# Performance work log

Measured on AMD Instinct MI355X. Metric: run time of the kernel, lower is better.

Reference implementation:

```python
import jax, jax.numpy as jnp
import numpy as np

N_USERS = 50000
N_ENTITIES = 100000
CHANNEL = 64
N_FACTORS = 4
N_REL = 9  # n_relations; weight has N_REL-1 rows
N_EDGES = 1_500_000
NNZ = 800_000
N_HOPS = 2


def _l2_normalize(x, eps=1e-12):
    # matches torch F.normalize(dim=1)
    n = jnp.sqrt(jnp.sum(x * x, axis=1, keepdims=True))
    return x / jnp.maximum(n, eps)


def _distance_correlation(t1, t2):
    # t1, t2: [d] rows of disen_weight_att (d = n_relations-1)
    ch = t1.shape[0]
    t1 = t1[:, None]
    t2 = t2[:, None]
    a_ = (t1 @ t1.T) * 2.0
    b_ = (t2 @ t2.T) * 2.0
    t1s = t1 ** 2
    t2s = t2 ** 2
    a = jnp.sqrt(jnp.maximum(t1s - a_ + t1s.T, 0.0) + 1e-8)
    b = jnp.sqrt(jnp.maximum(t2s - b_ + t2s.T, 0.0) + 1e-8)
    A = a - a.mean(axis=0, keepdims=True) - a.mean(axis=1, keepdims=True) + a.mean()
    B = b - b.mean(axis=0, keepdims=True) - b.mean(axis=1, keepdims=True) + b.mean()
    dcov_AB = jnp.sqrt(jnp.maximum((A * B).sum() / ch ** 2, 0.0) + 1e-8)
    dcov_AA = jnp.sqrt(jnp.maximum((A * A).sum() / ch ** 2, 0.0) + 1e-8)
    dcov_BB = jnp.sqrt(jnp.maximum((B * B).sum() / ch ** 2, 0.0) + 1e-8)
    return dcov_AB / jnp.sqrt(dcov_AA * dcov_BB + 1e-8)


def _cul_cor(disen_weight_att):
    cor = jnp.asarray(0.0, disen_weight_att.dtype)
    for i in range(N_FACTORS):
        for j in range(i + 1, N_FACTORS):
            cor = cor + _distance_correlation(disen_weight_att[i], disen_weight_att[j])
    return cor


def setup_inputs() -> dict:
    key = jax.random.key(0)
    ks = jax.random.split(key, 11)
    return {
        "user_emb": jax.random.normal(ks[0], (N_USERS, CHANNEL), jnp.float32) * 0.1,
        "entity_emb": jax.random.normal(ks[1], (N_ENTITIES, CHANNEL), jnp.float32) * 0.1,
        "latent_emb": jax.random.normal(ks[2], (N_FACTORS, CHANNEL), jnp.float32) * 0.1,
        "weight": jax.random.normal(ks[3], (N_REL - 1, CHANNEL), jnp.float32) * 0.1,
        "disen_weight_att": jax.random.normal(ks[4], (N_FACTORS, N_REL - 1), jnp.float32) * 0.1,
        "interact_vals": jax.random.uniform(ks[5], (NNZ,), jnp.float32),
        "head": jax.random.randint(ks[6], (N_EDGES,), 0, N_ENTITIES),
        "tail": jax.random.randint(ks[7], (N_EDGES,), 0, N_ENTITIES),
        "edge_type": jax.random.randint(ks[8], (N_EDGES,), 1, N_REL),  # in [1, N_REL-1]
        "interact_rows": jax.random.randint(ks[9], (NNZ,), 0, N_USERS),
        "interact_cols": jax.random.randint(ks[10], (NNZ,), 0, N_ENTITIES),
    }


def reference(user_emb, entity_emb, latent_emb, weight, disen_weight_att,
              interact_vals, head, tail, edge_type, interact_rows, interact_cols):
    n_entities = entity_emb.shape[0]
    n_users = user_emb.shape[0]
    cor = _cul_cor(disen_weight_att)

    entity_res = entity_emb
    user_res = user_emb
    ones_e = jnp.ones((head.shape[0],), entity_emb.dtype)
    cnt = jax.ops.segment_sum(ones_e, head, num_segments=n_entities)  # reused: head fixed
    cnt = jnp.maximum(cnt, 1.0)[:, None]

    for _ in range(N_HOPS):
        # KG aggregate: gather tail emb * relation emb, scatter-mean by head
        rel_emb = weight[edge_type - 1]                      # [E, C]
        msg = entity_emb[tail] * rel_emb                     # [E, C]
        entity_agg = jax.ops.segment_sum(msg, head, num_segments=n_entities) / cnt

        # user -> latent factor attention
        score = jax.nn.softmax(user_emb @ latent_emb.T, axis=1)   # [U, F]

        # user aggregate: sparse.mm(interact_mat, entity_emb)
        gathered = interact_vals[:, None] * entity_emb[interact_cols]  # [nnz, C]
        user_agg = jax.ops.segment_sum(gathered, interact_rows, num_segments=n_users)

        disen_weight = jax.nn.softmax(disen_weight_att, axis=-1) @ weight  # [F, C]
        mix = score @ disen_weight                                          # [U, C]
        user_new = user_agg * mix + user_agg

        entity_emb = _l2_normalize(entity_agg)
        user_emb = _l2_normalize(user_new)
        entity_res = entity_res + entity_emb
        user_res = user_res + user_emb

    return entity_res, user_res, cor
```

## Files before the change

kernel.cpp:

```cpp
#include <hip/hip_runtime.h>
#include <math.h>

constexpr int CH         = 64;
constexpr int N_USERS    = 50000;
constexpr int N_ENTITIES = 100000;
constexpr int N_FACTORS  = 4;
constexpr int N_RELM1    = 8;
constexpr int N_EDGES    = 1500000;
constexpr int NNZ        = 800000;

constexpr int NBE        = (N_ENTITIES + 255) / 256;
constexpr int NBU        = (N_USERS + 255) / 256;
constexpr int NBKT       = NBE + NBU;
constexpr int TOTAL      = N_EDGES + NNZ;
constexpr int IPB        = 2048;
constexpr int NBLK       = (TOTAL + IPB - 1) / IPB;
constexpr int ENT_BLK8   = N_ENTITIES / 8;
constexpr int USR_BLK8   = N_USERS / 8;

typedef unsigned int u32;
typedef float __attribute__((ext_vector_type(4))) f32x4;
typedef unsigned int __attribute__((ext_vector_type(4))) u32x4;

__device__ __forceinline__ u32 pack_bf16x2(float a, float b) {
    u32 ua = __float_as_uint(a), ub = __float_as_uint(b);
    u32 ra = (ua + 0x7FFFu + ((ua >> 16) & 1u)) >> 16;
    u32 rb = (ub + 0x7FFFu + ((ub >> 16) & 1u)) >> 16;
    return ra | (rb << 16);
}
__device__ __forceinline__ float bf_lo(u32 v) { return __uint_as_float(v << 16); }
__device__ __forceinline__ float bf_hi(u32 v) { return __uint_as_float(v & 0xFFFF0000u); }

__device__ __forceinline__ float4 nt_ld4f(const float4* p) {
    f32x4 v = __builtin_nontemporal_load((const f32x4*)p);
    return make_float4(v.x, v.y, v.z, v.w);
}
__device__ __forceinline__ void nt_st4f(float4* p, float4 v) {
    f32x4 t; t.x = v.x; t.y = v.y; t.z = v.z; t.w = v.w;
    __builtin_nontemporal_store(t, (f32x4*)p);
}
__device__ __forceinline__ int   nt_ldi(const int* p)   { return __builtin_nontemporal_load(p); }
__device__ __forceinline__ float nt_ldf(const float* p) { return __builtin_nontemporal_load(p); }

__device__ __forceinline__ uint4 gz(const u32* __restrict__ t, int r, int c8, bool v) {
    uint4 x = make_uint4(0u, 0u, 0u, 0u);
    if (v) x = ((const uint4*)t)[r * 8 + c8];
    return x;
}

__device__ __forceinline__ int coarse_bucket(int i, const int* __restrict__ head,
                                             const int* __restrict__ irows) {
    return (i < N_EDGES) ? (head[i] >> 8) : (NBE + (irows[i - N_EDGES] >> 8));
}

__global__ __launch_bounds__(256)
void count_coarse(const int* __restrict__ head, const int* __restrict__ irows,
                  int* __restrict__ H) {
    __shared__ int hist[NBKT];
    for (int j = threadIdx.x; j < NBKT; j += 256) hist[j] = 0;
    __syncthreads();
    int start = blockIdx.x * IPB;
    int end   = min(start + IPB, TOTAL);
    for (int i = start + threadIdx.x; i < end; i += 256)
        atomicAdd(&hist[coarse_bucket(i, head, irows)], 1);
    __syncthreads();
    for (int j = threadIdx.x; j < NBKT; j += 256)
        H[j * NBLK + blockIdx.x] = hist[j];
}

__global__ __launch_bounds__(64)
void scan_hcols(int* __restrict__ H, int* __restrict__ T) {
    int b = blockIdx.x, lane = threadIdx.x;
    int carry = 0;
    for (int c = 0; c < (NBLK + 63) / 64; ++c) {
        int idx = c * 64 + lane;
        int v = (idx < NBLK) ? H[b * NBLK + idx] : 0;
        int incl = v;
        #pragma unroll
        for (int d = 1; d < 64; d <<= 1) {
            int u = __shfl_up(incl, d, 64);
            if (lane >= d) incl += u;
        }
        if (idx < NBLK) H[b * NBLK + idx] = carry + incl - v;
        carry += __shfl(incl, 63, 64);
    }
    if (lane == 0) T[b] = carry;
}

__global__ __launch_bounds__(1024)
void scan_buckets(const int* __restrict__ T, int* __restrict__ Bb) {
    __shared__ int lds[1024];
    int t = threadIdx.x;
    int v = (t < NBKT) ? T[t] : 0;
    lds[t] = v;
    __syncthreads();
    for (int d = 1; d < 1024; d <<= 1) {
        int u = (t >= d) ? lds[t - d] : 0;
        __syncthreads();
        lds[t] += u;
        __syncthreads();
    }
    if (t < NBKT) Bb[t] = lds[t] - v;
    if (t == NBKT - 1) Bb[NBKT] = lds[t];
}

__global__ __launch_bounds__(256)
void scatter_stage(const int* __restrict__ head, const int* __restrict__ tail,
                   const int* __restrict__ etype,
                   const int* __restrict__ irows, const int* __restrict__ icols,
                   const float* __restrict__ ivals,
                   const int* __restrict__ H, const int* __restrict__ Bb,
                   u32* __restrict__ stageE, u32* __restrict__ stageU,
                   float* __restrict__ stageUv) {
    __shared__ int cur[NBKT];
    for (int j = threadIdx.x; j < NBKT; j += 256)
        cur[j] = Bb[j] + H[j * NBLK + blockIdx.x];
    __syncthreads();
    int start = blockIdx.x * IPB;
    int end   = min(start + IPB, TOTAL);
    for (int i = start + threadIdx.x; i < end; i += 256) {
        if (i < N_EDGES) {
            int k   = head[i];
            u32 rec = (u32)tail[i] | ((u32)(etype[i] - 1) << 17) | ((u32)(k & 255) << 20);
            int pos = atomicAdd(&cur[k >> 8], 1);
            stageE[pos] = rec;
        } else {
            int ii  = i - N_EDGES;
            int k   = irows[ii];
            int pos = atomicAdd(&cur[NBE + (k >> 8)], 1) - N_EDGES;
            stageU[pos]  = (u32)icols[ii] | ((u32)(k & 255) << 17);
            stageUv[pos] = ivals[ii];
        }
    }
}

__global__ __launch_bounds__(256)
void bin_fill(const int* __restrict__ Bb,
              const u32* __restrict__ stageE, const u32* __restrict__ stageU,
              const float* __restrict__ stageUv,
              int* __restrict__ offE, int* __restrict__ offU,
              int* __restrict__ elst, int* __restrict__ ucol,
              float* __restrict__ uval) {
    __shared__ int khist[256];
    __shared__ int cur[256];
    int b = blockIdx.x, t = threadIdx.x;
    khist[t] = 0;
    __syncthreads();
    if (b < NBE) {
        int lo = Bb[b], hi = Bb[b + 1];
        for (int i = lo + t; i < hi; i += 256)
            atomicAdd(&khist[(stageE[i] >> 20) & 255], 1);
        __syncthreads();
        int v = khist[t];
        for (int d = 1; d < 256; d <<= 1) {
            int u = (t >= d) ? khist[t - d] : 0;
            __syncthreads();
            khist[t] += u;
            __syncthreads();
        }
        int excl = lo + khist[t] - v;
        int key  = b * 256 + t;
        if (key < N_ENTITIES) offE[key] = excl;
        cur[t] = excl;
        __syncthreads();
        for (int i = lo + t; i < hi; i += 256) {
            u32 s = stageE[i];
            int p = atomicAdd(&cur[(s >> 20) & 255], 1);
            elst[p] = (int)(s & 0xFFFFFu);
        }
        if (b == 0 && t == 0) offE[N_ENTITIES] = N_EDGES;
    } else {
        int lo = Bb[b] - N_EDGES, hi = Bb[b + 1] - N_EDGES;
        for (int i = lo + t; i < hi; i += 256)
            atomicAdd(&khist[(stageU[i] >> 17) & 255], 1);
        __syncthreads();
        int v = khist[t];
        for (int d = 1; d < 256; d <<= 1) {
            int u = (t >= d) ? khist[t - d] : 0;
            __syncthreads();
            khist[t] += u;
            __syncthreads();
        }
        int excl = lo + khist[t] - v;
        int key  = (b - NBE) * 256 + t;
        if (key < N_USERS) offU[key] = excl;
        cur[t] = excl;
        __syncthreads();
        for (int i = lo + t; i < hi; i += 256) {
            u32 s = stageU[i];
            float vv = stageUv[i];
            int p = atomicAdd(&cur[(s >> 17) & 255], 1);
            ucol[p] = (int)(s & 0x1FFFFu);
            uval[p] = vv;
        }
        if (b == NBE && t == 0) offU[N_USERS] = NNZ;
    }
}

__global__ __launch_bounds__(256)
void to_bf16(const float* __restrict__ src, u32* __restrict__ dst, int n2) {
    int i = blockIdx.x * 256 + threadIdx.x;
    if (i < n2) {
        float2 f = ((const float2*)src)[i];
        dst[i] = pack_bf16x2(f.x, f.y);
    }
}

__device__ __forceinline__ void acc_edge(float* acc, uint4 xv, float4 wa, float4 wb) {
    acc[0] += bf_lo(xv.x) * wa.x; acc[1] += bf_hi(xv.x) * wa.y;
    acc[2] += bf_lo(xv.y) * wa.z; acc[3] += bf_hi(xv.y) * wa.w;
    acc[4] += bf_lo(xv.z) * wb.x; acc[5] += bf_hi(xv.z) * wb.y;
    acc[6] += bf_lo(xv.w) * wb.z; acc[7] += bf_hi(xv.w) * wb.w;
}
__device__ __forceinline__ void acc_user(float* acc, uint4 xv, float vv) {
    acc[0] += vv * bf_lo(xv.x); acc[1] += vv * bf_hi(xv.x);
    acc[2] += vv * bf_lo(xv.y); acc[3] += vv * bf_hi(xv.y);
    acc[4] += vv * bf_lo(xv.z); acc[5] += vv * bf_hi(xv.z);
    acc[6] += vv * bf_lo(xv.w); acc[7] += vv * bf_hi(xv.w);
}

template <bool HOP0>
__global__ __launch_bounds__(256)
void hop_pass(const u32* __restrict__ entB,
              const float* __restrict__ usr_in,
              const float* __restrict__ weight, const float* __restrict__ latent,
              const float* __restrict__ dw,
              const int* __restrict__ offE, const int* __restrict__ elst,
              const int* __restrict__ offU, const int* __restrict__ ucol,
              const float* __restrict__ uval,
              u32* __restrict__ AeB_out,
              float* __restrict__ Au_out,
              float* __restrict__ ent_res, float* __restrict__ usr_res,
              const float* __restrict__ ent_base, const float* __restrict__ usr_base) {
    __shared__ float4 w4[N_RELM1 * 16];
    int lane = threadIdx.x & 63;
    int h    = lane >> 5;
    int g    = (lane >> 3) & 3;
    int c8   = lane & 7;
    int l5   = lane & 31;
    float acc[8] = {0.f, 0.f, 0.f, 0.f, 0.f, 0.f, 0.f, 0.f};

    if ((int)blockIdx.x < ENT_BLK8) {
        if (threadIdx.x < N_RELM1 * 16)
            w4[threadIdx.x] = ((const float4*)weight)[threadIdx.x];
        __syncthreads();
        int row = blockIdx.x * 8 + ((threadIdx.x >> 6) << 1) + h;
        int lo = offE[row], hi = offE[row + 1];
        for (int k0 = lo; k0 < hi; k0 += 32) {
            int m = min(32, hi - k0);
            int p = nt_ldi(&elst[min(k0 + l5, N_EDGES - 1)]);
            for (int jj = 0; jj < m; jj += 16) {
                int j0 = jj + g;
                int q0 = __shfl(p, j0,      32);
                int q1 = __shfl(p, j0 + 4,  32);
                int q2 = __shfl(p, j0 + 8,  32);
                int q3 = __shfl(p, j0 + 12, 32);
                uint4 x0 = gz(entB, q0 & 0x1FFFF, c8, j0      < m);
                uint4 x1 = gz(entB, q1 & 0x1FFFF, c8, j0 + 4  < m);
                uint4 x2 = gz(entB, q2 & 0x1FFFF, c8, j0 + 8  < m);
                uint4 x3 = gz(entB, q3 & 0x1FFFF, c8, j0 + 12 < m);
                float4 wa0 = w4[(q0 >> 17) * 16 + (c8 << 1)];
                float4 wb0 = w4[(q0 >> 17) * 16 + (c8 << 1) + 1];
                float4 wa1 = w4[(q1 >> 17) * 16 + (c8 << 1)];
                float4 wb1 = w4[(q1 >> 17) * 16 + (c8 << 1) + 1];
                float4 wa2 = w4[(q2 >> 17) * 16 + (c8 << 1)];
                float4 wb2 = w4[(q2 >> 17) * 16 + (c8 << 1) + 1];
                float4 wa3 = w4[(q3 >> 17) * 16 + (c8 << 1)];
                float4 wb3 = w4[(q3 >> 17) * 16 + (c8 << 1) + 1];
                acc_edge(acc, x0, wa0, wb0);
                acc_edge(acc, x1, wa1, wb1);
                acc_edge(acc, x2, wa2, wb2);
                acc_edge(acc, x3, wa3, wb3);
            }
        }
        #pragma unroll
        for (int j = 0; j < 8; ++j) {
            acc[j] += __shfl_xor(acc[j], 8, 64);
            acc[j] += __shfl_xor(acc[j], 16, 64);
        }
        float s = 0.0f;
        #pragma unroll
        for (int j = 0; j < 8; ++j) s += acc[j] * acc[j];
        s += __shfl_xor(s, 1, 64);
        s += __shfl_xor(s, 2, 64);
        s += __shfl_xor(s, 4, 64);
        float inv = 1.0f / fmaxf(sqrtf(s), 1e-12f);
        if (g == 0) {
            float y0 = acc[0] * inv, y1 = acc[1] * inv, y2 = acc[2] * inv, y3 = acc[3] * inv;
            float y4 = acc[4] * inv, y5 = acc[5] * inv, y6 = acc[6] * inv, y7 = acc[7] * inv;
            int qi = row * 16 + (c8 << 1);
            if (HOP0) {
                uint4 pk;
                pk.x = pack_bf16x2(y0, y1); pk.y = pack_bf16x2(y2, y3);
                pk.z = pack_bf16x2(y4, y5); pk.w = pack_bf16x2(y6, y7);
                ((uint4*)AeB_out)[row * 8 + c8] = pk;
                float4 b0 = nt_ld4f(&((const float4*)ent_base)[qi]);
                float4 b1 = nt_ld4f(&((const float4*)ent_base)[qi + 1]);
                nt_st4f(&((float4*)ent_res)[qi],     make_float4(b0.x + y0, b0.y + y1, b0.z + y2, b0.w + y3));
                nt_st4f(&((float4*)ent_res)[qi + 1], make_float4(b1.x + y4, b1.y + y5, b1.z + y6, b1.w + y7));
            } else {
                float4 r0 = nt_ld4f(&((const float4*)ent_res)[qi]);
                float4 r1 = nt_ld4f(&((const float4*)ent_res)[qi + 1]);
                nt_st4f(&((float4*)ent_res)[qi],     make_float4(r0.x + y0, r0.y + y1, r0.z + y2, r0.w + y3));
                nt_st4f(&((float4*)ent_res)[qi + 1], make_float4(r1.x + y4, r1.y + y5, r1.z + y6, r1.w + y7));
            }
        }
    } else {
        int row = (blockIdx.x - ENT_BLK8) * 8 + ((threadIdx.x >> 6) << 1) + h;
        int qi  = row * 16 + (c8 << 1);
        float4 u0 = nt_ld4f(&((const float4*)usr_in)[qi]);
        float4 u1 = nt_ld4f(&((const float4*)usr_in)[qi + 1]);
        int lo = offU[row], hi = offU[row + 1];
        for (int k0 = lo; k0 < hi; k0 += 32) {
            int m = min(32, hi - k0);
            int sidx = min(k0 + l5, NNZ - 1);
            int   cl = nt_ldi(&ucol[sidx]);
            float vl = nt_ldf(&uval[sidx]);
            for (int jj = 0; jj < m; jj += 16) {
                int j0 = jj + g;
                int   c0 = __shfl(cl, j0,      32);
                int   c1 = __shfl(cl, j0 + 4,  32);
                int   c2 = __shfl(cl, j0 + 8,  32);
                int   c3 = __shfl(cl, j0 + 12, 32);
                float v0 = __shfl(vl, j0,      32);
                float v1 = __shfl(vl, j0 + 4,  32);
                float v2 = __shfl(vl, j0 + 8,  32);
                float v3 = __shfl(vl, j0 + 12, 32);
                uint4 x0 = gz(entB, c0, c8, j0      < m);
                uint4 x1 = gz(entB, c1, c8, j0 + 4  < m);
                uint4 x2 = gz(entB, c2, c8, j0 + 8  < m);
                uint4 x3 = gz(entB, c3, c8, j0 + 12 < m);
                acc_user(acc, x0, v0);
                acc_user(acc, x1, v1);
                acc_user(acc, x2, v2);
                acc_user(acc, x3, v3);
            }
        }
        #pragma unroll
        for (int j = 0; j < 8; ++j) {
            acc[j] += __shfl_xor(acc[j], 8, 64);
            acc[j] += __shfl_xor(acc[j], 16, 64);
        }
        float d[N_FACTORS];
        #pragma unroll
        for (int f = 0; f < N_FACTORS; ++f) {
            float4 l0 = ((const float4*)latent)[f * 16 + (c8 << 1)];
            float4 l1 = ((const float4*)latent)[f * 16 + (c8 << 1) + 1];
            d[f] = u0.x * l0.x + u0.y * l0.y + u0.z * l0.z + u0.w * l0.w
                 + u1.x * l1.x + u1.y * l1.y + u1.z * l1.z + u1.w * l1.w;
            d[f] += __shfl_xor(d[f], 1, 64);
            d[f] += __shfl_xor(d[f], 2, 64);
            d[f] += __shfl_xor(d[f], 4, 64);
        }
        float mx = fmaxf(fmaxf(d[0], d[1]), fmaxf(d[2], d[3]));
        float ex0 = expf(d[0] - mx), ex1 = expf(d[1] - mx);
        float ex2 = expf(d[2] - mx), ex3 = expf(d[3] - mx);
        float sinv = 1.0f / (ex0 + ex1 + ex2 + ex3);
        float mix[8] = {0.f, 0.f, 0.f, 0.f, 0.f, 0.f, 0.f, 0.f};
        {
            float exf[N_FACTORS] = {ex0, ex1, ex2, ex3};
            #pragma unroll
            for (int f = 0; f < N_FACTORS; ++f) {
                float4 w0 = ((const float4*)dw)[f * 16 + (c8 << 1)];
                float4 w1 = ((const float4*)dw)[f * 16 + (c8 << 1) + 1];
                float ef = exf[f];
                mix[0] += ef * w0.x; mix[1] += ef * w0.y;
                mix[2] += ef * w0.z; mix[3] += ef * w0.w;
                mix[4] += ef * w1.x; mix[5] += ef * w1.y;
                mix[6] += ef * w1.z; mix[7] += ef * w1.w;
            }
            #pragma unroll
            for (int j = 0; j < 8; ++j) mix[j] *= sinv;
        }
        float un[8];
        #pragma unroll
        for (int j = 0; j < 8; ++j) un[j] = acc[j] * (1.0f + mix[j]);
        float s = 0.0f;
        #pragma unroll
        for (int j = 0; j < 8; ++j) s += un[j] * un[j];
        s += __shfl_xor(s, 1, 64);
        s += __shfl_xor(s, 2, 64);
        s += __shfl_xor(s, 4, 64);
        float inv = 1.0f / fmaxf(sqrtf(s), 1e-12f);
        if (g == 0) {
            float y0 = un[0] * inv, y1 = un[1] * inv, y2 = un[2] * inv, y3 = un[3] * inv;
            float y4 = un[4] * inv, y5 = un[5] * inv, y6 = un[6] * inv, y7 = un[7] * inv;
            if (HOP0) {
                nt_st4f(&((float4*)Au_out)[qi],     make_float4(y0, y1, y2, y3));
                nt_st4f(&((float4*)Au_out)[qi + 1], make_float4(y4, y5, y6, y7));
            } else {
                float4 b0 = nt_ld4f(&((const float4*)usr_base)[qi]);
                float4 b1 = nt_ld4f(&((const float4*)usr_base)[qi + 1]);
                nt_st4f(&((float4*)usr_res)[qi],
                        make_float4((b0.x + u0.x) + y0, (b0.y + u0.y) + y1,
                                    (b0.z + u0.z) + y2, (b0.w + u0.w) + y3));
                nt_st4f(&((float4*)usr_res)[qi + 1],
                        make_float4((b1.x + u1.x) + y4, (b1.y + u1.y) + y5,
                                    (b1.z + u1.z) + y6, (b1.w + u1.w) + y7));
            }
        }
    }
}

__global__ __launch_bounds__(384)
void discor_kernel(const float* __restrict__ att,
                   const float* __restrict__ weight,
                   float* __restrict__ dw,
                   float* __restrict__ cor_out) {
    __shared__ float part[6];
    if (blockIdx.x == 0) {
        if (threadIdx.x < 256) {
            int f = threadIdx.x >> 6;
            int c = threadIdx.x & 63;
            float m = -1e30f;
            #pragma unroll
            for (int j = 0; j < N_RELM1; ++j) m = fmaxf(m, att[f * N_RELM1 + j]);
            float s = 0.0f, w[N_RELM1];
            #pragma unroll
            for (int j = 0; j < N_RELM1; ++j) { w[j] = expf(att[f * N_RELM1 + j] - m); s += w[j]; }
            float acc = 0.0f;
            #pragma unroll
            for (int j = 0; j < N_RELM1; ++j) acc += w[j] * weight[j * CH + c];
            dw[f * CH + c] = acc / s;
        }
    } else {
        int w    = threadIdx.x >> 6;
        int lane = threadIdx.x & 63;
        const int pi[6] = {0, 0, 0, 1, 1, 2};
        const int pj[6] = {1, 2, 3, 2, 3, 3};
        int r = lane >> 3, c = lane & 7;
        const float* t1 = att + pi[w] * N_RELM1;
        const float* t2 = att + pj[w] * N_RELM1;
        float a  = sqrtf(fmaxf(t1[r] * t1[r] - 2.0f * t1[r] * t1[c] + t1[c] * t1[c], 0.0f) + 1e-8f);
        float bb = sqrtf(fmaxf(t2[r] * t2[r] - 2.0f * t2[r] * t2[c] + t2[c] * t2[c], 0.0f) + 1e-8f);
        float rsA = a, rsB = bb;
        #pragma unroll
        for (int o = 1; o < 8; o <<= 1) { rsA += __shfl_xor(rsA, o, 64); rsB += __shfl_xor(rsB, o, 64); }
        float csA = a, csB = bb;
        #pragma unroll
        for (int o = 8; o < 64; o <<= 1) { csA += __shfl_xor(csA, o, 64); csB += __shfl_xor(csB, o, 64); }
        float totA = rsA, totB = rsB;
        #pragma unroll
        for (int o = 8; o < 64; o <<= 1) { totA += __shfl_xor(totA, o, 64); totB += __shfl_xor(totB, o, 64); }
        float A = a  - csA * 0.125f - rsA * 0.125f + totA * (1.0f / 64.0f);
        float B = bb - csB * 0.125f - rsB * 0.125f + totB * (1.0f / 64.0f);
        float sAB = A * B, sAA = A * A, sBB = B * B;
        #pragma unroll
        for (int o = 1; o < 64; o <<= 1) {
            sAB += __shfl_xor(sAB, o, 64);
            sAA += __shfl_xor(sAA, o, 64);
            sBB += __shfl_xor(sBB, o, 64);
        }
        if (lane == 0) {
            float dAB = sqrtf(fmaxf(sAB * (1.0f / 64.0f), 0.0f) + 1e-8f);
            float dAA = sqrtf(fmaxf(sAA * (1.0f / 64.0f), 0.0f) + 1e-8f);
            float dBB = sqrtf(fmaxf(sBB * (1.0f / 64.0f), 0.0f) + 1e-8f);
            part[w] = dAB / sqrtf(dAA * dBB + 1e-8f);
        }
        __syncthreads();
        if (threadIdx.x == 0) {
            float s = 0.0f;
            for (int q = 0; q < 6; ++q) s += part[q];
            cor_out[0] = s;
        }
    }
}

extern "C" void kernel_launch(void* const* d_in, const int* in_sizes, int n_in,
                              void* d_out, int out_size, void* d_ws, size_t ws_size,
                              hipStream_t stream) {
    const float* user_emb   = (const float*)d_in[0];
    const float* entity_emb = (const float*)d_in[1];
    const float* latent     = (const float*)d_in[2];
    const float* weight     = (const float*)d_in[3];
    const float* att        = (const float*)d_in[4];
    const float* ivals      = (const float*)d_in[5];
    const int*   head       = (const int*)d_in[6];
    const int*   tail       = (const int*)d_in[7];
    const int*   etype      = (const int*)d_in[8];
    const int*   irows      = (const int*)d_in[9];
    const int*   icols      = (const int*)d_in[10];

    float* out     = (float*)d_out;
    float* ent_res = out;
    float* usr_res = out + (size_t)N_ENTITIES * CH;
    float* cor_out = out + (size_t)N_ENTITIES * CH + (size_t)N_USERS * CH;

    const size_t ENT_ELEMS = (size_t)N_ENTITIES * CH;
    const size_t USR_ELEMS = (size_t)N_USERS * CH;
    const int    ENT_PAIRS = (int)(ENT_ELEMS / 2);

    float* ws   = (float*)d_ws;
    u32*   entB = (u32*)ws;
    u32*   AeB  = entB + ENT_PAIRS;
    float* Au   = (float*)(AeB + ENT_PAIRS);
    float* dw   = Au + USR_ELEMS;
    int*   offE = (int*)(dw + N_FACTORS * CH);
    int*   offU = offE + N_ENTITIES + 1;
    int*   elst = offU + N_USERS + 1;
    int*   ucol = elst + N_EDGES;
    float* uval = (float*)(ucol + NNZ);
    int*   H    = (int*)Au;
    int*   T    = H + NBKT * NBLK;
    int*   Bb   = T + NBKT;
    u32*   stageE  = entB;
    u32*   stageU  = entB + N_EDGES;
    float* stageUv = (float*)(stageU + NNZ);

    discor_kernel<<<2, 384, 0, stream>>>(att, weight, dw, cor_out);

    count_coarse<<<NBLK, 256, 0, stream>>>(head, irows, H);
    scan_hcols<<<NBKT, 64, 0, stream>>>(H, T);
    scan_buckets<<<1, 1024, 0, stream>>>(T, Bb);
    scatter_stage<<<NBLK, 256, 0, stream>>>(head, tail, etype, irows, icols, ivals,
                                            H, Bb, stageE, stageU, stageUv);
    bin_fill<<<NBKT, 256, 0, stream>>>(Bb, stageE, stageU, stageUv,
                                       offE, offU, elst, ucol, uval);

    to_bf16<<<(ENT_PAIRS + 255) / 256, 256, 0, stream>>>(entity_emb, entB, ENT_PAIRS);

    hop_pass<true><<<ENT_BLK8 + USR_BLK8, 256, 0, stream>>>(
        entB, user_emb, weight, latent, dw,
        offE, elst, offU, ucol, uval,
        AeB, Au, ent_res, usr_res, entity_emb, user_emb);

    hop_pass<false><<<ENT_BLK8 + USR_BLK8, 256, 0, stream>>>(
        AeB, Au, weight, latent, dw,
        offE, elst, offU, ucol, uval,
        nullptr, nullptr, ent_res, usr_res, entity_emb, user_emb);
}
```

Measured before the change: 347.9 us.

## Replace two-level bucketed CSR build with global-atomic count, scan, and scatter

```diff
diff --git a/kernel.cpp b/kernel.cpp
--- a/kernel.cpp
+++ b/kernel.cpp
@@ -13,14 +13,12 @@
 constexpr int NBU        = (N_USERS + 255) / 256;
 constexpr int NBKT       = NBE + NBU;
 constexpr int TOTAL      = N_EDGES + NNZ;
-constexpr int IPB        = 2048;
-constexpr int NBLK       = (TOTAL + IPB - 1) / IPB;
+constexpr int ITEM_BLKS  = (TOTAL + 255) / 256;
 constexpr int ENT_BLK8   = N_ENTITIES / 8;
 constexpr int USR_BLK8   = N_USERS / 8;
 
 typedef unsigned int u32;
 typedef float __attribute__((ext_vector_type(4))) f32x4;
-typedef unsigned int __attribute__((ext_vector_type(4))) u32x4;
 
 __device__ __forceinline__ u32 pack_bf16x2(float a, float b) {
     u32 ua = __float_as_uint(a), ub = __float_as_uint(b);
@@ -39,8 +37,6 @@
     f32x4 t; t.x = v.x; t.y = v.y; t.z = v.z; t.w = v.w;
     __builtin_nontemporal_store(t, (f32x4*)p);
 }
-__device__ __forceinline__ int   nt_ldi(const int* p)   { return __builtin_nontemporal_load(p); }
-__device__ __forceinline__ float nt_ldf(const float* p) { return __builtin_nontemporal_load(p); }
 
 __device__ __forceinline__ uint4 gz(const u32* __restrict__ t, int r, int c8, bool v) {
     uint4 x = make_uint4(0u, 0u, 0u, 0u);
@@ -48,50 +44,49 @@
     return x;
 }
 
-__device__ __forceinline__ int coarse_bucket(int i, const int* __restrict__ head,
-                                             const int* __restrict__ irows) {
-    return (i < N_EDGES) ? (head[i] >> 8) : (NBE + (irows[i - N_EDGES] >> 8));
-}
-
-__global__ __launch_bounds__(256)
-void count_coarse(const int* __restrict__ head, const int* __restrict__ irows,
-                  int* __restrict__ H) {
-    __shared__ int hist[NBKT];
-    for (int j = threadIdx.x; j < NBKT; j += 256) hist[j] = 0;
+
+__global__ __launch_bounds__(256)
+void count_direct(const int* __restrict__ head, const int* __restrict__ irows,
+                  int* __restrict__ curE, int* __restrict__ curU) {
+    int i = blockIdx.x * 256 + threadIdx.x;
+    if (i >= TOTAL) return;
+    if (i < N_EDGES) atomicAdd(&curE[head[i]], 1);
+    else             atomicAdd(&curU[irows[i - N_EDGES]], 1);
+}
+
+__global__ __launch_bounds__(256)
+void scan_blocks(const int* __restrict__ curE, const int* __restrict__ curU,
+                 int* __restrict__ offE, int* __restrict__ offU,
+                 int* __restrict__ T) {
+    __shared__ int wsum[4];
+    int b = blockIdx.x, t = threadIdx.x;
+    int w = t >> 6, lane = t & 63;
+    int key, limit;
+    const int* cnt;
+    int* off;
+    if (b < NBE) { key = b * 256 + t;         limit = N_ENTITIES; cnt = curE; off = offE; }
+    else         { key = (b - NBE) * 256 + t; limit = N_USERS;    cnt = curU; off = offU; }
+    int v = (key < limit) ? cnt[key] : 0;
+    int incl = v;
+    #pragma unroll
+    for (int d = 1; d < 64; d <<= 1) {
+        int u = __shfl_up(incl, d, 64);
+        if (lane >= d) incl += u;
+    }
+    if (lane == 63) wsum[w] = incl;
     __syncthreads();
-    int start = blockIdx.x * IPB;
-    int end   = min(start + IPB, TOTAL);
-    for (int i = start + threadIdx.x; i < end; i += 256)
-        atomicAdd(&hist[coarse_bucket(i, head, irows)], 1);
-    __syncthreads();
-    for (int j = threadIdx.x; j < NBKT; j += 256)
-        H[j * NBLK + blockIdx.x] = hist[j];
-}
-
-__global__ __launch_bounds__(64)
-void scan_hcols(int* __restrict__ H, int* __restrict__ T) {
-    int b = blockIdx.x, lane = threadIdx.x;
-    int carry = 0;
-    for (int c = 0; c < (NBLK + 63) / 64; ++c) {
-        int idx = c * 64 + lane;
-        int v = (idx < NBLK) ? H[b * NBLK + idx] : 0;
-        int incl = v;
-        #pragma unroll
-        for (int d = 1; d < 64; d <<= 1) {
-            int u = __shfl_up(incl, d, 64);
-            if (lane >= d) incl += u;
-        }
-        if (idx < NBLK) H[b * NBLK + idx] = carry + incl - v;
-        carry += __shfl(incl, 63, 64);
-    }
-    if (lane == 0) T[b] = carry;
+    int base = 0;
+    #pragma unroll
+    for (int q = 0; q < 4; ++q) if (q < w) base += wsum[q];
+    if (key < limit) off[key] = base + incl - v;
+    if (t == 255) T[b] = base + incl;
 }
 
 __global__ __launch_bounds__(1024)
-void scan_buckets(const int* __restrict__ T, int* __restrict__ Bb) {
+void scan_T(const int* __restrict__ T, int* __restrict__ Bb) {
     __shared__ int lds[1024];
     int t = threadIdx.x;
-    int v = (t < NBKT) ? T[t] : 0;
+    int v = (t < NBE) ? T[t] : 0;
     lds[t] = v;
     __syncthreads();
     for (int d = 1; d < 1024; d <<= 1) {
@@ -100,100 +95,62 @@
         lds[t] += u;
         __syncthreads();
     }
-    if (t < NBKT) Bb[t] = lds[t] - v;
-    if (t == NBKT - 1) Bb[NBKT] = lds[t];
-}
-
-__global__ __launch_bounds__(256)
-void scatter_stage(const int* __restrict__ head, const int* __restrict__ tail,
-                   const int* __restrict__ etype,
-                   const int* __restrict__ irows, const int* __restrict__ icols,
-                   const float* __restrict__ ivals,
-                   const int* __restrict__ H, const int* __restrict__ Bb,
-                   u32* __restrict__ stageE, u32* __restrict__ stageU,
-                   float* __restrict__ stageUv) {
-    __shared__ int cur[NBKT];
-    for (int j = threadIdx.x; j < NBKT; j += 256)
-        cur[j] = Bb[j] + H[j * NBLK + blockIdx.x];
+    if (t < NBE) Bb[t] = lds[t] - v;
     __syncthreads();
-    int start = blockIdx.x * IPB;
-    int end   = min(start + IPB, TOTAL);
-    for (int i = start + threadIdx.x; i < end; i += 256) {
-        if (i < N_EDGES) {
-            int k   = head[i];
-            u32 rec = (u32)tail[i] | ((u32)(etype[i] - 1) << 17) | ((u32)(k & 255) << 20);
-            int pos = atomicAdd(&cur[k >> 8], 1);
-            stageE[pos] = rec;
-        } else {
-            int ii  = i - N_EDGES;
-            int k   = irows[ii];
-            int pos = atomicAdd(&cur[NBE + (k >> 8)], 1) - N_EDGES;
-            stageU[pos]  = (u32)icols[ii] | ((u32)(k & 255) << 17);
-            stageUv[pos] = ivals[ii];
-        }
-    }
-}
-
-__global__ __launch_bounds__(256)
-void bin_fill(const int* __restrict__ Bb,
-              const u32* __restrict__ stageE, const u32* __restrict__ stageU,
-              const float* __restrict__ stageUv,
-              int* __restrict__ offE, int* __restrict__ offU,
-              int* __restrict__ elst, int* __restrict__ ucol,
-              float* __restrict__ uval) {
-    __shared__ int khist[256];
-    __shared__ int cur[256];
+    int v2 = (t < NBU) ? T[NBE + t] : 0;
+    lds[t] = v2;
+    __syncthreads();
+    for (int d = 1; d < 1024; d <<= 1) {
+        int u = (t >= d) ? lds[t - d] : 0;
+        __syncthreads();
+        lds[t] += u;
+        __syncthreads();
+    }
+    if (t < NBU) Bb[NBE + t] = lds[t] - v2;
+}
+
+__global__ __launch_bounds__(256)
+void addback(int* __restrict__ offE, int* __restrict__ offU,
+             int* __restrict__ curE, int* __restrict__ curU,
+             const int* __restrict__ Bb) {
     int b = blockIdx.x, t = threadIdx.x;
-    khist[t] = 0;
-    __syncthreads();
     if (b < NBE) {
-        int lo = Bb[b], hi = Bb[b + 1];
-        for (int i = lo + t; i < hi; i += 256)
-            atomicAdd(&khist[(stageE[i] >> 20) & 255], 1);
-        __syncthreads();
-        int v = khist[t];
-        for (int d = 1; d < 256; d <<= 1) {
-            int u = (t >= d) ? khist[t - d] : 0;
-            __syncthreads();
-            khist[t] += u;
-            __syncthreads();
-        }
-        int excl = lo + khist[t] - v;
-        int key  = b * 256 + t;
-        if (key < N_ENTITIES) offE[key] = excl;
-        cur[t] = excl;
-        __syncthreads();
-        for (int i = lo + t; i < hi; i += 256) {
-            u32 s = stageE[i];
-            int p = atomicAdd(&cur[(s >> 20) & 255], 1);
-            elst[p] = (int)(s & 0xFFFFFu);
+        int key = b * 256 + t;
+        if (key < N_ENTITIES) {
+            int o = offE[key] + Bb[b];
+            offE[key] = o;
+            curE[key] = o;
         }
         if (b == 0 && t == 0) offE[N_ENTITIES] = N_EDGES;
     } else {
-        int lo = Bb[b] - N_EDGES, hi = Bb[b + 1] - N_EDGES;
-        for (int i = lo + t; i < hi; i += 256)
-            atomicAdd(&khist[(stageU[i] >> 17) & 255], 1);
-        __syncthreads();
-        int v = khist[t];
-        for (int d = 1; d < 256; d <<= 1) {
-            int u = (t >= d) ? khist[t - d] : 0;
-            __syncthreads();
-            khist[t] += u;
-            __syncthreads();
-        }
-        int excl = lo + khist[t] - v;
-        int key  = (b - NBE) * 256 + t;
-        if (key < N_USERS) offU[key] = excl;
-        cur[t] = excl;
-        __syncthreads();
-        for (int i = lo + t; i < hi; i += 256) {
-            u32 s = stageU[i];
-            float vv = stageUv[i];
-            int p = atomicAdd(&cur[(s >> 17) & 255], 1);
-            ucol[p] = (int)(s & 0x1FFFFu);
-            uval[p] = vv;
+        int key = (b - NBE) * 256 + t;
+        if (key < N_USERS) {
+            int o = offU[key] + Bb[b];
+            offU[key] = o;
+            curU[key] = o;
         }
         if (b == NBE && t == 0) offU[N_USERS] = NNZ;
+    }
+}
+
+__global__ __launch_bounds__(256)
+void scatter_fill(const int* __restrict__ head, const int* __restrict__ tail,
+                  const int* __restrict__ etype,
+                  const int* __restrict__ irows, const int* __restrict__ icols,
+                  const float* __restrict__ ivals,
+                  int* __restrict__ curE, int* __restrict__ curU,
+                  int* __restrict__ elst, int* __restrict__ ucol,
+                  float* __restrict__ uval) {
+    int i = blockIdx.x * 256 + threadIdx.x;
+    if (i >= TOTAL) return;
+    if (i < N_EDGES) {
+        int p = atomicAdd(&curE[head[i]], 1);
+        elst[p] = tail[i] | ((etype[i] - 1) << 17);
+    } else {
+        int ii = i - N_EDGES;
+        int p = atomicAdd(&curU[irows[ii]], 1);
+        ucol[p] = icols[ii];
+        uval[p] = ivals[ii];
     }
 }
 
@@ -248,7 +205,7 @@
         int lo = offE[row], hi = offE[row + 1];
         for (int k0 = lo; k0 < hi; k0 += 32) {
             int m = min(32, hi - k0);
-            int p = nt_ldi(&elst[min(k0 + l5, N_EDGES - 1)]);
+            int p = elst[min(k0 + l5, N_EDGES - 1)];
             for (int jj = 0; jj < m; jj += 16) {
                 int j0 = jj + g;
                 int q0 = __shfl(p, j0,      32);
@@ -314,8 +271,8 @@
         for (int k0 = lo; k0 < hi; k0 += 32) {
             int m = min(32, hi - k0);
             int sidx = min(k0 + l5, NNZ - 1);
-            int   cl = nt_ldi(&ucol[sidx]);
-            float vl = nt_ldf(&uval[sidx]);
+            int   cl = ucol[sidx];
+            float vl = uval[sidx];
             for (int jj = 0; jj < m; jj += 16) {
                 int j0 = jj + g;
                 int   c0 = __shfl(cl, j0,      32);
@@ -500,22 +457,20 @@
     int*   elst = offU + N_USERS + 1;
     int*   ucol = elst + N_EDGES;
     float* uval = (float*)(ucol + NNZ);
-    int*   H    = (int*)Au;
-    int*   T    = H + NBKT * NBLK;
+    int*   curE = (int*)Au;
+    int*   curU = curE + N_ENTITIES;
+    int*   T    = curU + N_USERS;
     int*   Bb   = T + NBKT;
-    u32*   stageE  = entB;
-    u32*   stageU  = entB + N_EDGES;
-    float* stageUv = (float*)(stageU + NNZ);
 
     discor_kernel<<<2, 384, 0, stream>>>(att, weight, dw, cor_out);
 
-    count_coarse<<<NBLK, 256, 0, stream>>>(head, irows, H);
-    scan_hcols<<<NBKT, 64, 0, stream>>>(H, T);
-    scan_buckets<<<1, 1024, 0, stream>>>(T, Bb);
-    scatter_stage<<<NBLK, 256, 0, stream>>>(head, tail, etype, irows, icols, ivals,
-                                            H, Bb, stageE, stageU, stageUv);
-    bin_fill<<<NBKT, 256, 0, stream>>>(Bb, stageE, stageU, stageUv,
-                                       offE, offU, elst, ucol, uval);
+    hipMemsetAsync(curE, 0, (size_t)(N_ENTITIES + N_USERS) * sizeof(int), stream);
+    count_direct<<<ITEM_BLKS, 256, 0, stream>>>(head, irows, curE, curU);
+    scan_blocks<<<NBKT, 256, 0, stream>>>(curE, curU, offE, offU, T);
+    scan_T<<<1, 1024, 0, stream>>>(T, Bb);
+    addback<<<NBKT, 256, 0, stream>>>(offE, offU, curE, curU, Bb);
+    scatter_fill<<<ITEM_BLKS, 256, 0, stream>>>(head, tail, etype, irows, icols, ivals,
+                                                curE, curU, elst, ucol, uval);
 
     to_bf16<<<(ENT_PAIRS + 255) / 256, 256, 0, stream>>>(entity_emb, entB, ENT_PAIRS);
 
```

Result: slower. 530.3 us (+52.4%).
